# Optimization experiments

Hardware: AMD Instinct MI355X
Metric: run time of the kernel (lower is better)

The kernel has to match this reference:

```python
import jax, jax.numpy as jnp
import numpy as np

DIM = 256
NUM_LAYERS = 64


def setup_inputs() -> dict:
    key = jax.random.key(0)
    kx, kt = jax.random.split(key)
    x = jax.random.normal(kx, (32768, DIM), dtype=jnp.float32)
    # theta[l, p]: scalar angle for pair p in layer l. Odd-offset layers use only
    # the first DIM//2 - 1 entries. Matches torch.randn(()) * pi init.
    theta = jax.random.normal(kt, (NUM_LAYERS, DIM // 2), dtype=jnp.float32) * jnp.pi
    return {"x": x, "theta": theta}


def _apply_layer(x, th, offset):
    """Apply one layer of 2x2 Givens-like rotations to pairs (i, i+1).

    U = [[c, s], [s, -c]] with c=cos(2*theta), s=sin(2*theta); U is symmetric so
    out = vec @ U.T = vec @ U -> yi = c*xi + s*xj, yj = s*xi - c*xj.
    """
    b, d = x.shape
    if offset == 0:
        npairs = d // 2
        c = jnp.cos(2.0 * th[:npairs])  # [npairs]
        s = jnp.sin(2.0 * th[:npairs])
        v = x.reshape(b, npairs, 2)
        xi, xj = v[..., 0], v[..., 1]
        yi = c * xi + s * xj
        yj = s * xi - c * xj
        return jnp.stack([yi, yj], axis=-1).reshape(b, d)
    else:
        npairs = d // 2 - 1
        c = jnp.cos(2.0 * th[:npairs])
        s = jnp.sin(2.0 * th[:npairs])
        inner = x[:, 1:d - 1].reshape(b, npairs, 2)
        xi, xj = inner[..., 0], inner[..., 1]
        yi = c * xi + s * xj
        yj = s * xi - c * xj
        mid = jnp.stack([yi, yj], axis=-1).reshape(b, d - 2)
        return jnp.concatenate([x[:, :1], mid, x[:, d - 1:]], axis=1)


def reference(x, theta):
    # Python loop over num_layers (fixed, small structural set).
    for depth in range(NUM_LAYERS):
        x = _apply_layer(x, theta[depth], depth % 2)
    return x
```

## Files before the change

kernel.cpp:

```cpp
#include <hip/hip_runtime.h>
#include <math.h>

#define DIM 256
#define NLAYERS 64

typedef __attribute__((ext_vector_type(8))) short short8;
typedef __attribute__((ext_vector_type(4))) float f32x4;

__device__ __forceinline__ float dpp_shl1_zero(float v) {
    int r = __builtin_amdgcn_update_dpp(0, __float_as_int(v), 0x130, 0xF, 0xF, true);
    return __int_as_float(r);
}
__device__ __forceinline__ float dpp_shr1_keep(float oldv, float v) {
    int r = __builtin_amdgcn_update_dpp(__float_as_int(oldv), __float_as_int(v), 0x138, 0xF, 0xF, false);
    return __int_as_float(r);
}
__device__ __forceinline__ unsigned short f2bf(float f) {
    unsigned u = __float_as_uint(f);
    u += 0x7FFFu + ((u >> 16) & 1u);
    return (unsigned short)(u >> 16);
}
__device__ __forceinline__ unsigned cvtpk_bf16(float a, float b) {
    unsigned r;
    asm("v_cvt_pk_bf16_f32 %0, %1, %2" : "=v"(r) : "v"(a), "v"(b));
    return r;
}

__global__ __launch_bounds__(256)
void build_m_kernel(const float* __restrict__ theta, unsigned short* __restrict__ bfrag) {
    __shared__ float tbl[NLAYERS * DIM];
    const int tid = threadIdx.x;
    #pragma unroll 4
    for (int kk = 0; kk < 32; ++kk) {
        int idx = tid + 256 * kk;
        int l = idx >> 7, p = idx & 127;
        float a = 2.0f * theta[idx];
        float s = __sinf(a), c = __cosf(a);
        if ((l & 1) && (p == 127)) { c = 1.0f; s = 0.0f; }
        tbl[idx * 2 + 0] = c;
        tbl[idx * 2 + 1] = s;
    }
    __syncthreads();

    const int w = tid >> 6;
    const int t = tid & 63;
    const int row = blockIdx.x * 4 + w;

    float e[4];
    #pragma unroll
    for (int j = 0; j < 4; ++j) e[j] = (4 * t + j == row) ? 1.0f : 0.0f;

    const float4* tbl4 = (const float4*)tbl;
    #pragma unroll 2
    for (int l = 0; l < NLAYERS; l += 2) {
        float4 cs = tbl4[(l << 6) + t];
        {
            float a0 = e[0], a1 = e[1], a2 = e[2], a3 = e[3];
            e[0] = cs.x * a0 + cs.y * a1;
            e[1] = cs.y * a0 - cs.x * a1;
            e[2] = cs.z * a2 + cs.w * a3;
            e[3] = cs.w * a2 - cs.z * a3;
        }
        float4 cs1 = tbl4[((l + 1) << 6) + t];
        {
            float a1 = e[1], a2 = e[2], a3 = e[3];
            float n1 = cs1.x * a1 + cs1.y * a2;
            float n2 = cs1.y * a1 - cs1.x * a2;
            float xjn = dpp_shl1_zero(e[0]);
            float n3  = cs1.z * a3 + cs1.w * xjn;
            float snd = cs1.w * a3 - cs1.z * xjn;
            e[0] = dpp_shr1_keep(e[0], snd);
            e[1] = n1; e[2] = n2; e[3] = n3;
        }
    }

    const int kt = row >> 5, g8 = (row >> 3) & 3, ki = row & 7;
    #pragma unroll
    for (int j = 0; j < 4; ++j) {
        int col = 4 * t + j;
        bfrag[(((col >> 4) * 8 + kt) * 64 + g8 * 16 + (col & 15)) * 8 + ki] = f2bf(e[j]);
    }
}

__global__ __launch_bounds__(512, 4)
void clements_gemm(const float* __restrict__ x,
                   const unsigned short* __restrict__ bfrag,
                   float* __restrict__ out) {
    __shared__ float axf[4][16][64][4];

    const int tid = threadIdx.x;
    const int w   = tid >> 6;
    const int t   = tid & 63;
    const int l16 = t & 15;
    const int g   = t >> 4;
    const long rowbase = (long)blockIdx.x * 64;

    short8 Bf[8][2];
    {
        const short8* bp = (const short8*)bfrag;
        #pragma unroll
        for (int nt = 0; nt < 2; ++nt)
            #pragma unroll
            for (int kt = 0; kt < 8; ++kt)
                Bf[kt][nt] = bp[((w * 2 + nt) * 8 + kt) * 64 + t];
    }
    asm volatile("" ::: "memory");

    const int r0 = 2 * w, r1 = 2 * w + 1;
    const int gr0 = ((t & 48) | ((t ^ r0) & 15)) * 4;
    const int gr1 = ((t & 48) | ((t ^ r1) & 15)) * 4;

#define STAGE(i) { \
    const float* g0 = x + (rowbase + (i) * 16 + r0) * 256 + gr0; \
    const float* g1 = x + (rowbase + (i) * 16 + r1) * 256 + gr1; \
    __builtin_amdgcn_global_load_lds((const __attribute__((address_space(1))) void*)g0, \
        (__attribute__((address_space(3))) void*)&axf[i][r0][0][0], 16, 0, 0); \
    __builtin_amdgcn_global_load_lds((const __attribute__((address_space(1))) void*)g1, \
        (__attribute__((address_space(3))) void*)&axf[i][r1][0][0], 16, 0, 0); }

#define GATE(n) { asm volatile("s_waitcnt vmcnt(" #n ")" ::: "memory"); \
                  __builtin_amdgcn_s_barrier(); \
                  __builtin_amdgcn_sched_barrier(0); }

    auto compute = [&](int i) {
        f32x4 a0 = {0.f,0.f,0.f,0.f}, a1 = {0.f,0.f,0.f,0.f};
        #pragma unroll
        for (int kt = 0; kt < 8; ++kt) {
            int j0 = kt * 8 + g * 2;
            int s0 = (j0 & 48) | ((j0 ^ l16) & 15);
            int s1 = ((j0 + 1) & 48) | (((j0 + 1) ^ l16) & 15);
            f32x4 f0 = *(const f32x4*)&axf[i][l16][s0][0];
            f32x4 f1 = *(const f32x4*)&axf[i][l16][s1][0];
            union { short8 s; unsigned u[4]; } A;
            A.u[0] = cvtpk_bf16(f0[0], f0[1]);
            A.u[1] = cvtpk_bf16(f0[2], f0[3]);
            A.u[2] = cvtpk_bf16(f1[0], f1[1]);
            A.u[3] = cvtpk_bf16(f1[2], f1[3]);
            a0 = __builtin_amdgcn_mfma_f32_16x16x32_bf16(A.s, Bf[kt][0], a0, 0, 0, 0);
            a1 = __builtin_amdgcn_mfma_f32_16x16x32_bf16(A.s, Bf[kt][1], a1, 0, 0, 0);
        }
        float* o = out + (rowbase + i * 16 + g * 4) * 256 + 32 * w + l16;
        #pragma unroll
        for (int j = 0; j < 4; ++j) {
            o[(long)j * 256 +  0] = a0[j];
            o[(long)j * 256 + 16] = a1[j];
        }
    };

    STAGE(0) STAGE(1) STAGE(2)

    GATE(4)  STAGE(3) compute(0);
    GATE(12) compute(1);
    GATE(18) compute(2);
    GATE(16) compute(3);
#undef STAGE
#undef GATE
}

__global__ __launch_bounds__(1024, 4)
void clements_direct(const float* __restrict__ x,
                     const float* __restrict__ theta,
                     float* __restrict__ out) {
    __shared__ float tbl[NLAYERS * DIM];
    const int tid = threadIdx.x;
    #pragma unroll
    for (int k = 0; k < 8; ++k) {
        int idx = tid + 1024 * k;
        int l = idx >> 7;
        int p = idx & 127;
        float s, c;
        sincosf(2.0f * theta[idx], &s, &c);
        if ((l & 1) && (p == 127)) { c = 1.0f; s = 0.0f; }
        tbl[idx * 2 + 0] = c;
        tbl[idx * 2 + 1] = s;
    }
    __syncthreads();
    const int w = tid >> 6;
    const int t = tid & 63;
    const long base = ((long)blockIdx.x * 16 + w) * 8;
    float e[8][4];
    #pragma unroll
    for (int r = 0; r < 8; ++r) {
        float4 v = ((const float4*)(x + (base + r) * (long)DIM))[t];
        e[r][0] = v.x; e[r][1] = v.y; e[r][2] = v.z; e[r][3] = v.w;
    }
    const float4* tbl4 = (const float4*)tbl;
    #pragma unroll 2
    for (int l = 0; l < NLAYERS; l += 2) {
        float4 cs = tbl4[(l << 6) + t];
        #pragma unroll
        for (int r = 0; r < 8; ++r) {
            float a0 = e[r][0], a1 = e[r][1], a2 = e[r][2], a3 = e[r][3];
            e[r][0] = cs.x * a0 + cs.y * a1;
            e[r][1] = cs.y * a0 - cs.x * a1;
            e[r][2] = cs.z * a2 + cs.w * a3;
            e[r][3] = cs.w * a2 - cs.z * a3;
        }
        float4 cs1 = tbl4[((l + 1) << 6) + t];
        #pragma unroll
        for (int r = 0; r < 8; ++r) {
            float a1 = e[r][1], a2 = e[r][2], a3 = e[r][3];
            float n1 = cs1.x * a1 + cs1.y * a2;
            float n2 = cs1.y * a1 - cs1.x * a2;
            float xjn = dpp_shl1_zero(e[r][0]);
            float n3  = cs1.z * a3 + cs1.w * xjn;
            float snd = cs1.w * a3 - cs1.z * xjn;
            e[r][0] = dpp_shr1_keep(e[r][0], snd);
            e[r][1] = n1; e[r][2] = n2; e[r][3] = n3;
        }
    }
    #pragma unroll
    for (int r = 0; r < 8; ++r) {
        float4 v;
        v.x = e[r][0]; v.y = e[r][1]; v.z = e[r][2]; v.w = e[r][3];
        ((float4*)(out + (base + r) * (long)DIM))[t] = v;
    }
}

extern "C" void kernel_launch(void* const* d_in, const int* in_sizes, int n_in,
                              void* d_out, int out_size, void* d_ws, size_t ws_size,
                              hipStream_t stream) {
    const float* x     = (const float*)d_in[0];
    const float* theta = (const float*)d_in[1];
    float* out = (float*)d_out;

    const size_t need = (size_t)DIM * DIM * sizeof(unsigned short);
    if (ws_size >= need) {
        unsigned short* bfrag = (unsigned short*)d_ws;
        hipLaunchKernelGGL(build_m_kernel, dim3(64),  dim3(256), 0, stream, theta, bfrag);
        hipLaunchKernelGGL(clements_gemm,  dim3(512), dim3(512), 0, stream, x, bfrag, out);
    } else {
        hipLaunchKernelGGL(clements_direct, dim3(256), dim3(1024), 0, stream, x, theta, out);
    }
}
```

Before: 24.05 us.

## Load A fragments directly from global memory instead of staging via LDS

Removes the shared-memory staging of x tiles, along with the async global-to-LDS copies and barriers. Each wave now reads its A fragments straight from global memory, with a one-step register prefetch inside the k-loop. This drops the LDS footprint and synchronisation, but every wave in the block re-reads the same x rows. That multiplies global/cache read traffic and leaves less latency hiding across row tiles.

```diff
diff --git a/kernel.cpp b/kernel.cpp
--- a/kernel.cpp
+++ b/kernel.cpp
@@ -86,8 +86,6 @@
 void clements_gemm(const float* __restrict__ x,
                    const unsigned short* __restrict__ bfrag,
                    float* __restrict__ out) {
-    __shared__ float axf[4][16][64][4];
-
     const int tid = threadIdx.x;
     const int w   = tid >> 6;
     const int t   = tid & 63;
@@ -104,57 +102,39 @@
             for (int kt = 0; kt < 8; ++kt)
                 Bf[kt][nt] = bp[((w * 2 + nt) * 8 + kt) * 64 + t];
     }
-    asm volatile("" ::: "memory");
-
-    const int r0 = 2 * w, r1 = 2 * w + 1;
-    const int gr0 = ((t & 48) | ((t ^ r0) & 15)) * 4;
-    const int gr1 = ((t & 48) | ((t ^ r1) & 15)) * 4;
-
-#define STAGE(i) { \
-    const float* g0 = x + (rowbase + (i) * 16 + r0) * 256 + gr0; \
-    const float* g1 = x + (rowbase + (i) * 16 + r1) * 256 + gr1; \
-    __builtin_amdgcn_global_load_lds((const __attribute__((address_space(1))) void*)g0, \
-        (__attribute__((address_space(3))) void*)&axf[i][r0][0][0], 16, 0, 0); \
-    __builtin_amdgcn_global_load_lds((const __attribute__((address_space(1))) void*)g1, \
-        (__attribute__((address_space(3))) void*)&axf[i][r1][0][0], 16, 0, 0); }
-
-#define GATE(n) { asm volatile("s_waitcnt vmcnt(" #n ")" ::: "memory"); \
-                  __builtin_amdgcn_s_barrier(); \
-                  __builtin_amdgcn_sched_barrier(0); }
-
-    auto compute = [&](int i) {
-        f32x4 a0 = {0.f,0.f,0.f,0.f}, a1 = {0.f,0.f,0.f,0.f};
+
+    #pragma unroll
+    for (int rt = 0; rt < 4; ++rt) {
+        const float* xr = x + (rowbase + rt * 16 + l16) * 256 + g * 8;
+
+        f32x4 f0a = *(const f32x4*)(xr + 0);
+        f32x4 f0b = *(const f32x4*)(xr + 4);
+        f32x4 a0 = {0.f, 0.f, 0.f, 0.f}, a1 = {0.f, 0.f, 0.f, 0.f};
+
         #pragma unroll
         for (int kt = 0; kt < 8; ++kt) {
-            int j0 = kt * 8 + g * 2;
-            int s0 = (j0 & 48) | ((j0 ^ l16) & 15);
-            int s1 = ((j0 + 1) & 48) | (((j0 + 1) ^ l16) & 15);
-            f32x4 f0 = *(const f32x4*)&axf[i][l16][s0][0];
-            f32x4 f1 = *(const f32x4*)&axf[i][l16][s1][0];
+            f32x4 f1a, f1b;
+            if (kt < 7) {
+                f1a = *(const f32x4*)(xr + (kt + 1) * 32);
+                f1b = *(const f32x4*)(xr + (kt + 1) * 32 + 4);
+            }
             union { short8 s; unsigned u[4]; } A;
-            A.u[0] = cvtpk_bf16(f0[0], f0[1]);
-            A.u[1] = cvtpk_bf16(f0[2], f0[3]);
-            A.u[2] = cvtpk_bf16(f1[0], f1[1]);
-            A.u[3] = cvtpk_bf16(f1[2], f1[3]);
+            A.u[0] = cvtpk_bf16(f0a[0], f0a[1]);
+            A.u[1] = cvtpk_bf16(f0a[2], f0a[3]);
+            A.u[2] = cvtpk_bf16(f0b[0], f0b[1]);
+            A.u[3] = cvtpk_bf16(f0b[2], f0b[3]);
             a0 = __builtin_amdgcn_mfma_f32_16x16x32_bf16(A.s, Bf[kt][0], a0, 0, 0, 0);
             a1 = __builtin_amdgcn_mfma_f32_16x16x32_bf16(A.s, Bf[kt][1], a1, 0, 0, 0);
-        }
-        float* o = out + (rowbase + i * 16 + g * 4) * 256 + 32 * w + l16;
+            if (kt < 7) { f0a = f1a; f0b = f1b; }
+        }
+
+        float* o = out + (rowbase + rt * 16 + g * 4) * 256 + 32 * w + l16;
         #pragma unroll
         for (int j = 0; j < 4; ++j) {
             o[(long)j * 256 +  0] = a0[j];
             o[(long)j * 256 + 16] = a1[j];
         }
-    };
-
-    STAGE(0) STAGE(1) STAGE(2)
-
-    GATE(4)  STAGE(3) compute(0);
-    GATE(12) compute(1);
-    GATE(18) compute(2);
-    GATE(16) compute(3);
-#undef STAGE
-#undef GATE
+    }
 }
 
 __global__ __launch_bounds__(1024, 4)
```

Result: slower. 46.24 us (+92.3%).
